# Kernel tuning notes

Measured on AMD Instinct MI355X. Metric: run time of the kernel, lower is better.

Reference implementation:

```python
import jax, jax.numpy as jnp
import numpy as np

SIG_G = (1.0, 1.0, 1.0)  # Cl(3,0) metric signature -> 2^3 = 8 blades


def build_cayley(g):
    """Cayley table C[p, q, k] for the Clifford geometric product.
    Blades indexed by bitmasks; e_A * e_B = sign * metric * e_{A^B}."""
    n = len(g)
    nb = 1 << n
    C = np.zeros((nb, nb, nb), dtype=np.float32)
    for a in range(nb):
        for b in range(nb):
            # reordering sign: move generators of b past higher-index generators of a
            swaps = 0
            t = a >> 1
            while t:
                swaps += bin(t & b).count('1')
                t >>= 1
            s = -1.0 if (swaps & 1) else 1.0
            # metric contribution from repeated generators (e_i e_i = g_i)
            for i in range(n):
                if (a >> i) & 1 and (b >> i) & 1:
                    s *= g[i]
            C[a, b, a ^ b] = s
    return jnp.asarray(C)


def geometric_product(x, w, cayley):
    # x: [B, I, P blades], w: [O, I, Q blades] -> y: [B, O, K blades]
    return jnp.einsum('bip,oiq,pqk->bok', x, w, cayley)


def setup_inputs() -> dict:
    key = jax.random.key(0)
    kx, k1, k2, k3 = jax.random.split(key, 4)
    B, D, NB = 2048, 512, 8
    x = jax.random.normal(kx, (B, D, NB), dtype=jnp.float32)
    w1 = 0.1 * jax.random.normal(k1, (D, D, NB), dtype=jnp.float32)
    w2 = 0.1 * jax.random.normal(k2, (D, D, NB), dtype=jnp.float32)
    w3 = 0.1 * jax.random.normal(k3, (D, D, NB), dtype=jnp.float32)
    return {'x': x, 'w1': w1, 'w2': w2, 'w3': w3}


def reference(x, w1, w2, w3):
    cayley = build_cayley(SIG_G)  # [8, 8, 8], sparse Cayley table (constant)
    acts = [x]
    for w in (w1, w2, w3):
        acts.append(geometric_product(acts[-1], w, cayley))
    # original forward returns the list of activations; all share a shape here,
    # so stack to a single [L+1, B, D, NB] array
    return jnp.stack(acts, axis=0)
```

## Files before the change

### kernel.cpp

```cpp
#include <hip/hip_runtime.h>

using u16    = unsigned short;
using u32    = unsigned int;
using bf16x8 = __attribute__((ext_vector_type(8))) __bf16;
using f32x4  = __attribute__((ext_vector_type(4))) float;
using u16x4  = __attribute__((ext_vector_type(4))) u16;
using u16x8  = __attribute__((ext_vector_type(8))) u16;

__device__ __forceinline__ u16 f32_to_bf16(float f) {
    u32 u = __float_as_uint(f);
    u32 r = (u + 0x7FFFu + ((u >> 16) & 1u)) >> 16;
    return (u16)r;
}

__device__ __forceinline__ void gld_lds16(const void* g, void* l) {
    __builtin_amdgcn_global_load_lds(
        (const __attribute__((address_space(1))) u32*)g,
        (__attribute__((address_space(3))) u32*)l,
        16, 0, 0);
}

__device__ __forceinline__ float cl3_sign(int a, int b) {
    int swaps = __popc((a >> 1) & b) + __popc((a >> 2) & b);
    return (swaps & 1) ? -1.0f : 1.0f;
}

__global__ __launch_bounds__(256) void prep_kernel(
    const float* __restrict__ x, float* __restrict__ out0, u16* __restrict__ A0)
{
    const int t = blockIdx.x * 256 + threadIdx.x;
    const float4 v = reinterpret_cast<const float4*>(x)[t];
    reinterpret_cast<float4*>(out0)[t] = v;
    u16x4 b;
    b.x = f32_to_bf16(v.x);
    b.y = f32_to_bf16(v.y);
    b.z = f32_to_bf16(v.z);
    b.w = f32_to_bf16(v.w);
    reinterpret_cast<u16x4*>(A0)[t] = b;
}

__device__ __forceinline__ void expand_body(
    const float* __restrict__ w, u16* __restrict__ Wm, int t)
{
    const int o = t >> 9;
    const int i = t & 511;
    const float* src = w + ((size_t)t << 3);
    const float4 w0 = reinterpret_cast<const float4*>(src)[0];
    const float4 w1 = reinterpret_cast<const float4*>(src)[1];
    const float wv[8] = {w0.x, w0.y, w0.z, w0.w, w1.x, w1.y, w1.z, w1.w};
    #pragma unroll
    for (int kb = 0; kb < 8; ++kb) {
        u16x8 ov;
        #pragma unroll
        for (int p = 0; p < 8; ++p) {
            const int q = p ^ kb;
            ov[p] = f32_to_bf16(cl3_sign(p, q) * wv[q]);
        }
        reinterpret_cast<u16x8*>(Wm)[((size_t)(o * 8 + kb) << 9) + i] = ov;
    }
}

__global__ __launch_bounds__(256) void expand3_kernel(
    const float* __restrict__ wa, const float* __restrict__ wb,
    const float* __restrict__ wc,
    u16* __restrict__ Wa, u16* __restrict__ Wb, u16* __restrict__ Wc)
{
    const int bb = blockIdx.x;
    const int Lw = bb >> 10;
    const float* w = (Lw == 0) ? wa : (Lw == 1) ? wb : wc;
    u16* Wm       = (Lw == 0) ? Wa : (Lw == 1) ? Wb : Wc;
    expand_body(w, Wm, (bb & 1023) * 256 + threadIdx.x);
}

__global__ __launch_bounds__(256) void expand_kernel(
    const float* __restrict__ w, u16* __restrict__ Wm)
{
    expand_body(w, Wm, blockIdx.x * 256 + threadIdx.x);
}

constexpr int BM = 128, BN = 256, BK = 64, KDIM = 4096, NKT = KDIM / BK;
constexpr int ASZ = BM * BK;
constexpr int BSZ = BN * BK;
constexpr int BUF = ASZ + BSZ;

__global__ __launch_bounds__(512, 2) void gemm8_kernel(
    const u16* __restrict__ A,
    const u16* __restrict__ Bt,
    float*     __restrict__ C,
    u16*       __restrict__ An)
{
    __shared__ __attribute__((aligned(16))) u16 lds[3 * BUF];

    const int tid = threadIdx.x;
    const int l   = tid & 63;
    const int w   = tid >> 6;
    const int wr  = w >> 2;
    const int wc  = w & 3;
    const int l8  = l >> 3, l7 = l & 7;
    const int fr  = l & 15, fq = l >> 4;
    const int row0 = blockIdx.y * BM;
    const int col0 = blockIdx.x * BN;

    auto stageA = [&](int buf, int kt, int q) {
        const int r = (q * 8 + w) * 8 + l8;
        const u16* src = A + (size_t)(row0 + r) * KDIM + kt + ((l7 ^ l8) << 3);
        gld_lds16(src, &lds[buf * BUF + r * BK + l7 * 8]);
    };
    auto stageB = [&](int buf, int kt, int q) {
        const int r = (q * 8 + w) * 8 + l8;
        const u16* src = Bt + (size_t)(col0 + r) * KDIM + kt + ((l7 ^ l8) << 3);
        gld_lds16(src, &lds[buf * BUF + ASZ + r * BK + l7 * 8]);
    };
    auto rdA = [&](int buf, int mi, int ks) -> bf16x8 {
        const int r = wr * 64 + mi * 16 + fr;
        const int c = (ks * 4 + fq) ^ (r & 7);
        return *reinterpret_cast<const bf16x8*>(&lds[buf * BUF + r * BK + c * 8]);
    };
    auto rdB = [&](int buf, int ni, int ks) -> bf16x8 {
        const int r = wc * 64 + ni * 16 + fr;
        const int c = (ks * 4 + fq) ^ (r & 7);
        return *reinterpret_cast<const bf16x8*>(&lds[buf * BUF + ASZ + r * BK + c * 8]);
    };

    f32x4 acc[4][4];
    #pragma unroll
    for (int i = 0; i < 4; ++i)
        #pragma unroll
        for (int j = 0; j < 4; ++j)
            acc[i][j] = f32x4{0.f, 0.f, 0.f, 0.f};

    stageA(0, 0, 0); stageA(0, 0, 1);
    stageB(0, 0, 0); stageB(0, 0, 1); stageB(0, 0, 2); stageB(0, 0, 3);
    stageA(1, BK, 0); stageA(1, BK, 1);
    stageB(1, BK, 0); stageB(1, BK, 1); stageB(1, BK, 2); stageB(1, BK, 3);
    asm volatile("s_waitcnt vmcnt(6)" ::: "memory");
    __builtin_amdgcn_s_barrier();

    bf16x8 a[2][2], b[4][2];

    int cb = 0, nb = 2;
    for (int t = 0; t < NKT; ++t) {
        const int kt2 = (t + 2) * BK;
        const bool pre = (t + 2 < NKT);

        #pragma unroll
        for (int mi = 0; mi < 2; ++mi)
            #pragma unroll
            for (int ks = 0; ks < 2; ++ks) a[mi][ks] = rdA(cb, mi, ks);
        #pragma unroll
        for (int ni = 0; ni < 4; ++ni)
            #pragma unroll
            for (int ks = 0; ks < 2; ++ks) b[ni][ks] = rdB(cb, ni, ks);
        if (pre) { stageA(nb, kt2, 0); stageA(nb, kt2, 1); stageB(nb, kt2, 0); }
        __builtin_amdgcn_s_barrier();
        asm volatile("s_waitcnt lgkmcnt(0)" ::: "memory");
        __builtin_amdgcn_sched_barrier(0);
        __builtin_amdgcn_s_setprio(1);
        #pragma unroll
        for (int mi = 0; mi < 2; ++mi)
            #pragma unroll
            for (int ni = 0; ni < 4; ++ni)
                #pragma unroll
                for (int ks = 0; ks < 2; ++ks)
                    acc[mi][ni] = __builtin_amdgcn_mfma_f32_16x16x32_bf16(
                        a[mi][ks], b[ni][ks], acc[mi][ni], 0, 0, 0);
        __builtin_amdgcn_s_setprio(0);
        __builtin_amdgcn_s_barrier();

        #pragma unroll
        for (int mi = 0; mi < 2; ++mi)
            #pragma unroll
            for (int ks = 0; ks < 2; ++ks) a[mi][ks] = rdA(cb, mi + 2, ks);
        if (pre) { stageB(nb, kt2, 1); stageB(nb, kt2, 2); stageB(nb, kt2, 3); }
        __builtin_amdgcn_s_barrier();
        asm volatile("s_waitcnt lgkmcnt(0)" ::: "memory");
        __builtin_amdgcn_sched_barrier(0);
        __builtin_amdgcn_s_setprio(1);
        #pragma unroll
        for (int mi = 0; mi < 2; ++mi)
            #pragma unroll
            for (int ni = 0; ni < 4; ++ni)
                #pragma unroll
                for (int ks = 0; ks < 2; ++ks)
                    acc[mi + 2][ni] = __builtin_amdgcn_mfma_f32_16x16x32_bf16(
                        a[mi][ks], b[ni][ks], acc[mi + 2][ni], 0, 0, 0);
        __builtin_amdgcn_s_setprio(0);
        if (t + 2 < NKT)      { asm volatile("s_waitcnt vmcnt(6)" ::: "memory"); }
        else if (t + 1 < NKT) { asm volatile("s_waitcnt vmcnt(0)" ::: "memory"); }
        __builtin_amdgcn_s_barrier();

        cb = (cb == 2) ? 0 : cb + 1;
        nb = (nb == 2) ? 0 : nb + 1;
    }

    #pragma unroll
    for (int mi = 0; mi < 4; ++mi) {
        #pragma unroll
        for (int v = 0; v < 4; ++v) {
            const int r = row0 + wr * 64 + mi * 16 + fq * 4 + v;
            const size_t base = ((size_t)r << 12) + col0 + wc * 64 + fr;
            #pragma unroll
            for (int ni = 0; ni < 4; ++ni)
                C[base + ni * 16] = acc[mi][ni][v];
            if (An != nullptr) {
                #pragma unroll
                for (int ni = 0; ni < 4; ++ni)
                    An[base + ni * 16] = f32_to_bf16(acc[mi][ni][v]);
            }
        }
    }
}

extern "C" void kernel_launch(void* const* d_in, const int* in_sizes, int n_in,
                              void* d_out, int out_size, void* d_ws, size_t ws_size,
                              hipStream_t stream) {
    const float* x = (const float*)d_in[0];
    const float* wts[3] = {(const float*)d_in[1], (const float*)d_in[2],
                           (const float*)d_in[3]};
    float* out = (float*)d_out;

    constexpr size_t LAYER = (size_t)2048 * 4096;
    constexpr size_t WSZ   = (size_t)4096 * 4096;

    u16* A0 = (u16*)d_ws;
    u16* A1 = A0 + LAYER;

    prep_kernel<<<dim3(8192), dim3(256), 0, stream>>>(x, out, A0);

    const bool fused = ws_size >= (2 * LAYER + 3 * WSZ) * sizeof(u16);
    u16* Ac = A0;
    u16* Anx = A1;

    if (fused) {
        u16* Wm[3] = {A1 + LAYER, A1 + LAYER + WSZ, A1 + LAYER + 2 * WSZ};
        expand3_kernel<<<dim3(3072), dim3(256), 0, stream>>>(
            wts[0], wts[1], wts[2], Wm[0], Wm[1], Wm[2]);
        for (int L = 0; L < 3; ++L) {
            gemm8_kernel<<<dim3(16, 16), dim3(512), 0, stream>>>(
                Ac, Wm[L], out + (size_t)(L + 1) * LAYER, (L == 2) ? nullptr : Anx);
            u16* t = Ac; Ac = Anx; Anx = t;
        }
    } else {
        u16* Wm = A1 + LAYER;
        for (int L = 0; L < 3; ++L) {
            expand_kernel<<<dim3(1024), dim3(256), 0, stream>>>(wts[L], Wm);
            gemm8_kernel<<<dim3(16, 16), dim3(512), 0, stream>>>(
                Ac, Wm, out + (size_t)(L + 1) * LAYER, (L == 2) ? nullptr : Anx);
            u16* t = Ac; Ac = Anx; Anx = t;
        }
    }
}
```

Before: 421.9 us.

## Issue all prefetches upfront and use one barrier per GEMM k-iteration

```diff
diff --git a/kernel.cpp b/kernel.cpp
--- a/kernel.cpp
+++ b/kernel.cpp
@@ -39,9 +39,10 @@
     reinterpret_cast<u16x4*>(A0)[t] = b;
 }
 
-__device__ __forceinline__ void expand_body(
-    const float* __restrict__ w, u16* __restrict__ Wm, int t)
+__global__ __launch_bounds__(256) void expand_kernel(
+    const float* __restrict__ w, u16* __restrict__ Wm)
 {
+    const int t = blockIdx.x * 256 + threadIdx.x;
     const int o = t >> 9;
     const int i = t & 511;
     const float* src = w + ((size_t)t << 3);
@@ -60,24 +61,6 @@
     }
 }
 
-__global__ __launch_bounds__(256) void expand3_kernel(
-    const float* __restrict__ wa, const float* __restrict__ wb,
-    const float* __restrict__ wc,
-    u16* __restrict__ Wa, u16* __restrict__ Wb, u16* __restrict__ Wc)
-{
-    const int bb = blockIdx.x;
-    const int Lw = bb >> 10;
-    const float* w = (Lw == 0) ? wa : (Lw == 1) ? wb : wc;
-    u16* Wm       = (Lw == 0) ? Wa : (Lw == 1) ? Wb : Wc;
-    expand_body(w, Wm, (bb & 1023) * 256 + threadIdx.x);
-}
-
-__global__ __launch_bounds__(256) void expand_kernel(
-    const float* __restrict__ w, u16* __restrict__ Wm)
-{
-    expand_body(w, Wm, blockIdx.x * 256 + threadIdx.x);
-}
-
 constexpr int BM = 128, BN = 256, BK = 64, KDIM = 4096, NKT = KDIM / BK;
 constexpr int ASZ = BM * BK;
 constexpr int BSZ = BN * BK;
@@ -136,13 +119,17 @@
     asm volatile("s_waitcnt vmcnt(6)" ::: "memory");
     __builtin_amdgcn_s_barrier();
 
-    bf16x8 a[2][2], b[4][2];
-
     int cb = 0, nb = 2;
     for (int t = 0; t < NKT; ++t) {
         const int kt2 = (t + 2) * BK;
         const bool pre = (t + 2 < NKT);
 
+        if (pre) {
+            stageA(nb, kt2, 0); stageA(nb, kt2, 1);
+            stageB(nb, kt2, 0); stageB(nb, kt2, 1); stageB(nb, kt2, 2); stageB(nb, kt2, 3);
+        }
+
+        bf16x8 a[2][2], a2[2][2], b[4][2];
         #pragma unroll
         for (int mi = 0; mi < 2; ++mi)
             #pragma unroll
@@ -151,10 +138,12 @@
         for (int ni = 0; ni < 4; ++ni)
             #pragma unroll
             for (int ks = 0; ks < 2; ++ks) b[ni][ks] = rdB(cb, ni, ks);
-        if (pre) { stageA(nb, kt2, 0); stageA(nb, kt2, 1); stageB(nb, kt2, 0); }
-        __builtin_amdgcn_s_barrier();
-        asm volatile("s_waitcnt lgkmcnt(0)" ::: "memory");
+        #pragma unroll
+        for (int mi = 0; mi < 2; ++mi)
+            #pragma unroll
+            for (int ks = 0; ks < 2; ++ks) a2[mi][ks] = rdA(cb, mi + 2, ks);
         __builtin_amdgcn_sched_barrier(0);
+
         __builtin_amdgcn_s_setprio(1);
         #pragma unroll
         for (int mi = 0; mi < 2; ++mi)
@@ -165,16 +154,8 @@
                     acc[mi][ni] = __builtin_amdgcn_mfma_f32_16x16x32_bf16(
                         a[mi][ks], b[ni][ks], acc[mi][ni], 0, 0, 0);
         __builtin_amdgcn_s_setprio(0);
-        __builtin_amdgcn_s_barrier();
-
-        #pragma unroll
-        for (int mi = 0; mi < 2; ++mi)
-            #pragma unroll
-            for (int ks = 0; ks < 2; ++ks) a[mi][ks] = rdA(cb, mi + 2, ks);
-        if (pre) { stageB(nb, kt2, 1); stageB(nb, kt2, 2); stageB(nb, kt2, 3); }
-        __builtin_amdgcn_s_barrier();
-        asm volatile("s_waitcnt lgkmcnt(0)" ::: "memory");
         __builtin_amdgcn_sched_barrier(0);
+
         __builtin_amdgcn_s_setprio(1);
         #pragma unroll
         for (int mi = 0; mi < 2; ++mi)
@@ -183,8 +164,10 @@
                 #pragma unroll
                 for (int ks = 0; ks < 2; ++ks)
                     acc[mi + 2][ni] = __builtin_amdgcn_mfma_f32_16x16x32_bf16(
-                        a[mi][ks], b[ni][ks], acc[mi + 2][ni], 0, 0, 0);
+                        a2[mi][ks], b[ni][ks], acc[mi + 2][ni], 0, 0, 0);
         __builtin_amdgcn_s_setprio(0);
+        __builtin_amdgcn_sched_barrier(0);
+
         if (t + 2 < NKT)      { asm volatile("s_waitcnt vmcnt(6)" ::: "memory"); }
         else if (t + 1 < NKT) { asm volatile("s_waitcnt vmcnt(0)" ::: "memory"); }
         __builtin_amdgcn_s_barrier();
@@ -220,33 +203,19 @@
     float* out = (float*)d_out;
 
     constexpr size_t LAYER = (size_t)2048 * 4096;
-    constexpr size_t WSZ   = (size_t)4096 * 4096;
 
     u16* A0 = (u16*)d_ws;
     u16* A1 = A0 + LAYER;
+    u16* Wm = A1 + LAYER;
 
     prep_kernel<<<dim3(8192), dim3(256), 0, stream>>>(x, out, A0);
 
-    const bool fused = ws_size >= (2 * LAYER + 3 * WSZ) * sizeof(u16);
     u16* Ac = A0;
     u16* Anx = A1;
-
-    if (fused) {
-        u16* Wm[3] = {A1 + LAYER, A1 + LAYER + WSZ, A1 + LAYER + 2 * WSZ};
-        expand3_kernel<<<dim3(3072), dim3(256), 0, stream>>>(
-            wts[0], wts[1], wts[2], Wm[0], Wm[1], Wm[2]);
-        for (int L = 0; L < 3; ++L) {
-            gemm8_kernel<<<dim3(16, 16), dim3(512), 0, stream>>>(
-                Ac, Wm[L], out + (size_t)(L + 1) * LAYER, (L == 2) ? nullptr : Anx);
-            u16* t = Ac; Ac = Anx; Anx = t;
-        }
-    } else {
-        u16* Wm = A1 + LAYER;
-        for (int L = 0; L < 3; ++L) {
-            expand_kernel<<<dim3(1024), dim3(256), 0, stream>>>(wts[L], Wm);
-            gemm8_kernel<<<dim3(16, 16), dim3(512), 0, stream>>>(
-                Ac, Wm, out + (size_t)(L + 1) * LAYER, (L == 2) ? nullptr : Anx);
-            u16* t = Ac; Ac = Anx; Anx = t;
-        }
-    }
-}
+    for (int L = 0; L < 3; ++L) {
+        expand_kernel<<<dim3(1024), dim3(256), 0, stream>>>(wts[L], Wm);
+        gemm8_kernel<<<dim3(16, 16), dim3(512), 0, stream>>>(
+            Ac, Wm, out + (size_t)(L + 1) * LAYER, (L == 2) ? nullptr : Anx);
+        u16* t = Ac; Ac = Anx; Anx = t;
+    }
+}
```

Result: faster. 387.8 us (-8.1%).
